# Performance work log

Measured on AMD Instinct MI355X. Metric: run time of the kernel, lower is better.

The kernel has to match this reference:

```python
import jax, jax.numpy as jnp
import numpy as np

NUM_EMB = 512
EMB_DIM = 64
COMMIT = 0.25
DECAY = 0.99
EPS = 1e-05


def setup_inputs() -> dict:
    key = jax.random.key(0)
    k1, k2, k3 = jax.random.split(key, 3)
    inputs = jax.random.normal(k1, (EMB_DIM, 16, 8192), dtype=jnp.float32)  # [D, B, T]
    embedding = jax.random.normal(k2, (NUM_EMB, EMB_DIM), dtype=jnp.float32)
    ema_w = jax.random.normal(k3, (NUM_EMB, EMB_DIM), dtype=jnp.float32)
    ema_cluster_size = jnp.zeros((NUM_EMB,), dtype=jnp.float32)
    return {"inputs": inputs, "embedding": embedding, "ema_w": ema_w,
            "ema_cluster_size": ema_cluster_size}


def reference(inputs, embedding, ema_w, ema_cluster_size):
    # [D, B, T] -> [B, T, D]
    x = jnp.transpose(inputs, (1, 2, 0))
    in_shape = x.shape
    flat = x.reshape(-1, EMB_DIM)  # [N, D]

    # Squared L2 distances to every codebook entry: [N, K]
    distances = (jnp.sum(flat ** 2, axis=1, keepdims=True)
                 + jnp.sum(embedding ** 2, axis=1)
                 - 2.0 * flat @ embedding.T)
    idx = jnp.argmin(distances, axis=1)                       # [N]
    encodings = jax.nn.one_hot(idx, NUM_EMB, dtype=jnp.float32)  # [N, K]

    # EMA codebook update (training mode). torch wraps results in nn.Parameter,
    # which detaches them, so we stop_gradient the updated embedding.
    cluster = ema_cluster_size * DECAY + (1.0 - DECAY) * jnp.sum(encodings, axis=0)
    n = jnp.sum(cluster)
    cluster = (cluster + EPS) / (n + NUM_EMB * EPS) * n
    dw = jax.ops.segment_sum(flat, idx, num_segments=NUM_EMB)  # == encodings.T @ flat
    new_ema_w = ema_w * DECAY + (1.0 - DECAY) * dw
    new_emb = jax.lax.stop_gradient(new_ema_w / cluster[:, None])  # [K, D]

    # Quantize via gather (equivalent to encodings @ new_emb)
    quantized = new_emb[idx].reshape(in_shape)  # [B, T, D]

    e_latent_loss = jnp.mean((jax.lax.stop_gradient(quantized) - x) ** 2)
    loss = COMMIT * e_latent_loss

    # Straight-through estimator
    quantized_st = x + jax.lax.stop_gradient(quantized - x)

    avg_probs = jnp.mean(encodings, axis=0)
    perplexity = jnp.exp(-jnp.sum(avg_probs * jnp.log(avg_probs + 1e-10)))

    return (loss, jnp.transpose(quantized_st, (2, 0, 1)), perplexity, encodings, distances)
```

## Files before the change

### kernel.cpp

```cpp
#include <hip/hip_runtime.h>

#define NTOT 131072
#define KCB  512
#define DIM  64

__device__ __forceinline__ float wave_sum(float v) {
#pragma unroll
  for (int off = 32; off; off >>= 1) v += __shfl_xor(v, off, 64);
  return v;
}

__global__ __launch_bounds__(512, 2) void k_dist(
    const float* __restrict__ x_g,
    const float* __restrict__ emb_g,
    float* __restrict__ dist_out,
    float* __restrict__ enc_out,
    int* __restrict__ idx_out,
    unsigned* __restrict__ cnt_g,
    float* __restrict__ dw_g)
{
  __shared__ __align__(16) float embt[DIM][KCB];
  __shared__ __align__(16) float xls[8][8][65];
  __shared__ unsigned lcnt[KCB];

  const int t = threadIdx.x;
  const int lane = t & 63;
  const int w = t >> 6;

  lcnt[t] = 0u;

  {
    const float* er = emb_g + t * DIM;
#pragma unroll
    for (int d0 = 0; d0 < DIM; d0 += 4) {
      const float4 e = *reinterpret_cast<const float4*>(er + d0);
      embt[d0 + 0][t] = -2.f * e.x;
      embt[d0 + 1][t] = -2.f * e.y;
      embt[d0 + 2][t] = -2.f * e.z;
      embt[d0 + 3][t] = -2.f * e.w;
    }
  }
  __syncthreads();

  float ebr[8] = {0.f, 0.f, 0.f, 0.f, 0.f, 0.f, 0.f, 0.f};
  for (int d = 0; d < DIM; ++d) {
    const float4 a = *reinterpret_cast<const float4*>(&embt[d][4 * lane]);
    const float4 b = *reinterpret_cast<const float4*>(&embt[d][256 + 4 * lane]);
    ebr[0] = fmaf(a.x, a.x, ebr[0]); ebr[1] = fmaf(a.y, a.y, ebr[1]);
    ebr[2] = fmaf(a.z, a.z, ebr[2]); ebr[3] = fmaf(a.w, a.w, ebr[3]);
    ebr[4] = fmaf(b.x, b.x, ebr[4]); ebr[5] = fmaf(b.y, b.y, ebr[5]);
    ebr[6] = fmaf(b.z, b.z, ebr[6]); ebr[7] = fmaf(b.w, b.w, ebr[7]);
  }
#pragma unroll
  for (int j = 0; j < 8; ++j) ebr[j] *= 0.25f;

  const int nb = blockIdx.x * 512;
  const int r_own = lane & 7;
  const int dgc   = lane >> 3;

  float xv[8];
  {
    const int n0w = nb + w * 8;
#pragma unroll
    for (int j = 0; j < 8; ++j)
      xv[j] = x_g[(size_t)(dgc * 8 + j) * NTOT + n0w + r_own];
  }

  for (int tt = 0; tt < 8; ++tt) {
    const int n0w = nb + tt * 64 + w * 8;

    asm volatile("" ::: "memory");

#pragma unroll
    for (int j = 0; j < 8; ++j)
      xls[w][r_own][dgc * 8 + j] = xv[j];

    asm volatile("" ::: "memory");

    float ps = 0.f;
#pragma unroll
    for (int j = 0; j < 8; ++j) ps = fmaf(xv[j], xv[j], ps);
    ps += __shfl_xor(ps, 8, 64);
    ps += __shfl_xor(ps, 16, 64);
    ps += __shfl_xor(ps, 32, 64);

    float xr[8];
#pragma unroll
    for (int r = 0; r < 8; ++r) xr[r] = xls[w][r][lane];

    float acc[8][8];
#pragma unroll
    for (int r = 0; r < 8; ++r)
#pragma unroll
      for (int j = 0; j < 8; ++j) acc[r][j] = ebr[j];

#pragma unroll 2
    for (int d = 0; d < DIM; ++d) {
      const float4 e0 = *reinterpret_cast<const float4*>(&embt[d][4 * lane]);
      const float4 e1 = *reinterpret_cast<const float4*>(&embt[d][256 + 4 * lane]);
#pragma unroll
      for (int r = 0; r < 8; ++r) {
        const float s = __uint_as_float(
            __builtin_amdgcn_readlane(__float_as_uint(xr[r]), d));
        acc[r][0] = fmaf(s, e0.x, acc[r][0]);
        acc[r][1] = fmaf(s, e0.y, acc[r][1]);
        acc[r][2] = fmaf(s, e0.z, acc[r][2]);
        acc[r][3] = fmaf(s, e0.w, acc[r][3]);
        acc[r][4] = fmaf(s, e1.x, acc[r][4]);
        acc[r][5] = fmaf(s, e1.y, acc[r][5]);
        acc[r][6] = fmaf(s, e1.z, acc[r][6]);
        acc[r][7] = fmaf(s, e1.w, acc[r][7]);
      }
    }

    if (tt < 7) {
      const int n1w = nb + (tt + 1) * 64 + w * 8;
#pragma unroll
      for (int j = 0; j < 8; ++j)
        xv[j] = x_g[(size_t)(dgc * 8 + j) * NTOT + n1w + r_own];
    }
    asm volatile("" ::: "memory");

#pragma unroll
    for (int r = 0; r < 8; ++r) {
      const int nr = n0w + r;
      const float xs = __uint_as_float(
          __builtin_amdgcn_readlane(__float_as_uint(ps), r));
      float dv[8];
#pragma unroll
      for (int j = 0; j < 8; ++j) dv[j] = acc[r][j] + xs;

      unsigned long long best = ~0ull;
#pragma unroll
      for (int j = 0; j < 8; ++j) {
        const unsigned kk = (j < 4) ? (unsigned)(4 * lane + j)
                                    : (unsigned)(256 + 4 * lane + (j - 4));
        const unsigned long long pk =
            ((unsigned long long)__float_as_uint(dv[j]) << 32) | kk;
        best = pk < best ? pk : best;
      }
#pragma unroll
      for (int off = 32; off; off >>= 1) {
        const unsigned long long o = __shfl_xor(best, off, 64);
        best = o < best ? o : best;
      }
      const int kmin = (int)(best & 0xFFFFFFFFull);

      float* dp = dist_out + (size_t)nr * KCB + 4 * lane;
      float4 q;
      q.x = dv[0]; q.y = dv[1]; q.z = dv[2]; q.w = dv[3];
      *reinterpret_cast<float4*>(dp) = q;
      q.x = dv[4]; q.y = dv[5]; q.z = dv[6]; q.w = dv[7];
      *reinterpret_cast<float4*>(dp + 256) = q;

      float* ep = enc_out + (size_t)nr * KCB + 4 * lane;
      const int k0 = 4 * lane;
      float4 z;
      z.x = (kmin == k0)     ? 1.f : 0.f;
      z.y = (kmin == k0 + 1) ? 1.f : 0.f;
      z.z = (kmin == k0 + 2) ? 1.f : 0.f;
      z.w = (kmin == k0 + 3) ? 1.f : 0.f;
      *reinterpret_cast<float4*>(ep) = z;
      z.x = (kmin == 256 + k0)     ? 1.f : 0.f;
      z.y = (kmin == 256 + k0 + 1) ? 1.f : 0.f;
      z.z = (kmin == 256 + k0 + 2) ? 1.f : 0.f;
      z.w = (kmin == 256 + k0 + 3) ? 1.f : 0.f;
      *reinterpret_cast<float4*>(ep + 256) = z;

      if (lane == 0) {
        idx_out[nr] = kmin;
        atomicAdd(&lcnt[kmin], 1u);
      }
      unsafeAtomicAdd(dw_g + ((size_t)kmin << 6) + lane, xr[r]);
    }
  }

  __syncthreads();
  if (lcnt[t]) atomicAdd(&cnt_g[t], lcnt[t]);
}

__global__ __launch_bounds__(512, 1) void k_final(
    const float* __restrict__ ema_w, const float* __restrict__ ema_cs,
    const unsigned* __restrict__ cnt, const float* __restrict__ dw,
    float* __restrict__ nemb, float* __restrict__ out)
{
  __shared__ float red[8];
  __shared__ float bc;
  const int t = threadIdx.x;
  const int lane = t & 63, w = t >> 6;

  const float c = (float)cnt[t];
  const float craw = ema_cs[t] * 0.99f + 0.01f * c;

  float s = wave_sum(craw);
  if (lane == 0) red[w] = s;
  __syncthreads();
  if (t == 0) {
    float a = 0.f;
#pragma unroll
    for (int i = 0; i < 8; ++i) a += red[i];
    bc = a;
  }
  __syncthreads();
  const float n = bc;
  const float clus = (craw + 1e-5f) / (n + 512.f * 1e-5f) * n;

  const float4* wr = reinterpret_cast<const float4*>(ema_w + t * 64);
  const float4* dr = reinterpret_cast<const float4*>(dw + t * 64);
  float4* nr = reinterpret_cast<float4*>(nemb + t * 64);
#pragma unroll
  for (int q = 0; q < 16; ++q) {
    const float4 wv = wr[q], dv = dr[q];
    float4 o;
    o.x = (wv.x * 0.99f + 0.01f * dv.x) / clus;
    o.y = (wv.y * 0.99f + 0.01f * dv.y) / clus;
    o.z = (wv.z * 0.99f + 0.01f * dv.z) / clus;
    o.w = (wv.w * 0.99f + 0.01f * dv.w) / clus;
    nr[q] = o;
  }

  const float p = c * (1.f / 131072.f);
  const float term = p * logf(p + 1e-10f);
  float s2 = wave_sum(term);
  if (lane == 0) red[w] = s2;
  __syncthreads();
  if (t == 0) {
    float a = 0.f;
#pragma unroll
    for (int i = 0; i < 8; ++i) a += red[i];
    out[8388609] = expf(-a);
  }
}

__global__ __launch_bounds__(256, 4) void k_quant(
    const float* __restrict__ x_g, const int* __restrict__ idx_g,
    const float* __restrict__ nemb, float* __restrict__ out)
{
  float lsum = 0.f;
  const int stride = gridDim.x * 256;
  for (int i = blockIdx.x * 256 + threadIdx.x; i < (DIM * NTOT / 4); i += stride) {
    const int d = i >> 15;
    const int n4 = i & ((NTOT / 4) - 1);
    const float4 xv = *reinterpret_cast<const float4*>(x_g + ((size_t)d << 17) + 4 * n4);
    const int4 id = *reinterpret_cast<const int4*>(idx_g + 4 * n4);
    const float q0 = nemb[(id.x << 6) + d];
    const float q1 = nemb[(id.y << 6) + d];
    const float q2 = nemb[(id.z << 6) + d];
    const float q3 = nemb[(id.w << 6) + d];
    const float e0 = q0 - xv.x, e1 = q1 - xv.y, e2 = q2 - xv.z, e3 = q3 - xv.w;
    float* op = out + 1 + ((size_t)d << 17) + 4 * n4;
    op[0] = xv.x + e0;
    op[1] = xv.y + e1;
    op[2] = xv.z + e2;
    op[3] = xv.w + e3;
    lsum += e0 * e0 + e1 * e1 + e2 * e2 + e3 * e3;
  }
  lsum = wave_sum(lsum);
  __shared__ float wsum[4];
  const int lane = threadIdx.x & 63, w = threadIdx.x >> 6;
  if (lane == 0) wsum[w] = lsum;
  __syncthreads();
  if (threadIdx.x == 0)
    unsafeAtomicAdd(out, (wsum[0] + wsum[1] + wsum[2] + wsum[3]) * (0.25f / 8388608.f));
}

extern "C" void kernel_launch(void* const* d_in, const int* in_sizes, int n_in,
                              void* d_out, int out_size, void* d_ws, size_t ws_size,
                              hipStream_t stream) {
  const float* x      = (const float*)d_in[0];
  const float* emb    = (const float*)d_in[1];
  const float* ema_w  = (const float*)d_in[2];
  const float* ema_cs = (const float*)d_in[3];
  float* out = (float*)d_out;

  float* enc_out  = out + 8388610;
  float* dist_out = out + 75497474;

  char* ws = (char*)d_ws;
  float*    dw   = (float*)ws;
  unsigned* cnt  = (unsigned*)(ws + 131072);
  float*    nemb = (float*)(ws + 133120);
  int*      idx  = (int*)(ws + 264192);

  hipMemsetAsync(d_ws, 0, 133120, stream);
  hipMemsetAsync(d_out, 0, sizeof(float), stream);

  k_dist<<<256, 512, 0, stream>>>(x, emb, dist_out, enc_out, idx, cnt, dw);
  k_final<<<1, 512, 0, stream>>>(ema_w, ema_cs, cnt, dw, nemb, out);
  k_quant<<<2048, 256, 0, stream>>>(x, idx, nemb, out);
}
```

Measured before the change: 240.7 us.

## Precompute transposed codebook in a prep kernel and read it from global memory

Adds a small kernel that writes the -2-scaled transposed codebook and the squared norms to workspace. The distance kernel drops its 128KB shared-memory copy and instead streams codebook rows from global memory (cache) in its inner loop. It raises the occupancy hint from 2 to 3 blocks per CU. The aim is to remove the per-block staging and norm computation and to allow more resident blocks, at the cost of an extra launch and higher-latency cached global loads in the hot loop.

```diff
diff --git a/kernel.cpp b/kernel.cpp
--- a/kernel.cpp
+++ b/kernel.cpp
@@ -10,16 +10,31 @@
   return v;
 }
 
-__global__ __launch_bounds__(512, 2) void k_dist(
+__global__ __launch_bounds__(512, 1) void k_prep(
+    const float* __restrict__ emb, float* __restrict__ embT,
+    float* __restrict__ embsq)
+{
+  const int k = threadIdx.x;
+  float sq = 0.f;
+#pragma unroll 8
+  for (int d = 0; d < DIM; ++d) {
+    const float e = emb[k * DIM + d];
+    sq = fmaf(e, e, sq);
+    embT[d * KCB + k] = -2.f * e;
+  }
+  embsq[k] = sq;
+}
+
+__global__ __launch_bounds__(512, 3) void k_dist(
     const float* __restrict__ x_g,
-    const float* __restrict__ emb_g,
+    const float* __restrict__ embT,
+    const float* __restrict__ embsq,
     float* __restrict__ dist_out,
     float* __restrict__ enc_out,
     int* __restrict__ idx_out,
     unsigned* __restrict__ cnt_g,
     float* __restrict__ dw_g)
 {
-  __shared__ __align__(16) float embt[DIM][KCB];
   __shared__ __align__(16) float xls[8][8][65];
   __shared__ unsigned lcnt[KCB];
 
@@ -28,31 +43,11 @@
   const int w = t >> 6;
 
   lcnt[t] = 0u;
-
-  {
-    const float* er = emb_g + t * DIM;
-#pragma unroll
-    for (int d0 = 0; d0 < DIM; d0 += 4) {
-      const float4 e = *reinterpret_cast<const float4*>(er + d0);
-      embt[d0 + 0][t] = -2.f * e.x;
-      embt[d0 + 1][t] = -2.f * e.y;
-      embt[d0 + 2][t] = -2.f * e.z;
-      embt[d0 + 3][t] = -2.f * e.w;
-    }
-  }
-  __syncthreads();
-
-  float ebr[8] = {0.f, 0.f, 0.f, 0.f, 0.f, 0.f, 0.f, 0.f};
-  for (int d = 0; d < DIM; ++d) {
-    const float4 a = *reinterpret_cast<const float4*>(&embt[d][4 * lane]);
-    const float4 b = *reinterpret_cast<const float4*>(&embt[d][256 + 4 * lane]);
-    ebr[0] = fmaf(a.x, a.x, ebr[0]); ebr[1] = fmaf(a.y, a.y, ebr[1]);
-    ebr[2] = fmaf(a.z, a.z, ebr[2]); ebr[3] = fmaf(a.w, a.w, ebr[3]);
-    ebr[4] = fmaf(b.x, b.x, ebr[4]); ebr[5] = fmaf(b.y, b.y, ebr[5]);
-    ebr[6] = fmaf(b.z, b.z, ebr[6]); ebr[7] = fmaf(b.w, b.w, ebr[7]);
-  }
-#pragma unroll
-  for (int j = 0; j < 8; ++j) ebr[j] *= 0.25f;
+  __syncthreads();
+
+  const float4 eb0 = *reinterpret_cast<const float4*>(embsq + 4 * lane);
+  const float4 eb1 = *reinterpret_cast<const float4*>(embsq + 256 + 4 * lane);
+  float ebr[8] = {eb0.x, eb0.y, eb0.z, eb0.w, eb1.x, eb1.y, eb1.z, eb1.w};
 
   const int nb = blockIdx.x * 512;
   const int r_own = lane & 7;
@@ -96,8 +91,9 @@
 
 #pragma unroll 2
     for (int d = 0; d < DIM; ++d) {
-      const float4 e0 = *reinterpret_cast<const float4*>(&embt[d][4 * lane]);
-      const float4 e1 = *reinterpret_cast<const float4*>(&embt[d][256 + 4 * lane]);
+      const float* er = embT + d * KCB + 4 * lane;
+      const float4 e0 = *reinterpret_cast<const float4*>(er);
+      const float4 e1 = *reinterpret_cast<const float4*>(er + 256);
 #pragma unroll
       for (int r = 0; r < 8; ++r) {
         const float s = __uint_as_float(
@@ -277,15 +273,18 @@
   float* dist_out = out + 75497474;
 
   char* ws = (char*)d_ws;
-  float*    dw   = (float*)ws;
-  unsigned* cnt  = (unsigned*)(ws + 131072);
-  float*    nemb = (float*)(ws + 133120);
-  int*      idx  = (int*)(ws + 264192);
+  float*    dw    = (float*)ws;
+  unsigned* cnt   = (unsigned*)(ws + 131072);
+  float*    nemb  = (float*)(ws + 133120);
+  int*      idx   = (int*)(ws + 264192);
+  float*    embT  = (float*)(ws + 788480);
+  float*    embsq = (float*)(ws + 919552);
 
   hipMemsetAsync(d_ws, 0, 133120, stream);
   hipMemsetAsync(d_out, 0, sizeof(float), stream);
 
-  k_dist<<<256, 512, 0, stream>>>(x, emb, dist_out, enc_out, idx, cnt, dw);
+  k_prep<<<1, 512, 0, stream>>>(emb, embT, embsq);
+  k_dist<<<256, 512, 0, stream>>>(x, embT, embsq, dist_out, enc_out, idx, cnt, dw);
   k_final<<<1, 512, 0, stream>>>(ema_w, ema_cs, cnt, dw, nemb, out);
   k_quant<<<2048, 256, 0, stream>>>(x, idx, nemb, out);
 }
```

After: 274.9 us. 14.2% more time.
